# Kernel tuning notes

Hardware: AMD Instinct MI355X
Metric: run time of the kernel (lower is better)

## Reference

```python
import jax, jax.numpy as jnp
import numpy as np

NEG_SLOPE = 0.01  # torch F.leaky_relu default


def _sage_layer(src, dst, ew, x_src, num_dst, W_self, W_neigh, b):
    # x_src: [N_src, T, C]; messages m_e = w_e * x_src[src_e]  -> [E, T, C]
    msg = x_src[src] * ew[:, None, None]
    agg = jax.ops.segment_sum(msg, dst, num_segments=num_dst)  # [N_dst, T, C]
    x_dst = x_src[:num_dst]
    # self- and neighbor-linear (GraphSAGE): [N_dst, T, H]
    return (jnp.einsum('ntc,hc->nth', x_dst, W_self)
            + jnp.einsum('ntc,hc->nth', agg, W_neigh) + b)


def setup_inputs() -> dict:
    key = jax.random.key(0)
    ks = jax.random.split(key, 12)
    T, N_src1, C_in, H, C_out = 12, 50000, 32, 64, 32
    N_dst1, N_dst2 = 20000, 10000
    E1, E2 = 320000, 160000
    inp = {
        'node_feat': jax.random.normal(ks[0], (T, N_src1, C_in), jnp.float32),
        'src1': jax.random.randint(ks[1], (E1,), 0, N_src1),
        'dst1': jax.random.randint(ks[2], (E1,), 0, N_dst1),
        'ew1': jax.random.uniform(ks[3], (E1,), jnp.float32),
        'src2': jax.random.randint(ks[4], (E2,), 0, N_dst1),
        'dst2': jax.random.randint(ks[5], (E2,), 0, N_dst2),
        'ew2': jax.random.uniform(ks[6], (E2,), jnp.float32),
        'W1_self': jax.random.normal(ks[7], (H, C_in), jnp.float32) / np.sqrt(C_in),
        'W1_neigh': jax.random.normal(ks[8], (H, C_in), jnp.float32) / np.sqrt(C_in),
        'b1': jnp.zeros((H,), jnp.float32),
        'W2_self': jax.random.normal(ks[9], (C_out, H), jnp.float32) / np.sqrt(H),
        'W2_neigh': jax.random.normal(ks[10], (C_out, H), jnp.float32) / np.sqrt(H),
        'b2': jnp.zeros((C_out,), jnp.float32),
        'num_dst1': N_dst1,
        'num_dst2': N_dst2,
    }
    return inp


def reference(node_feat, src1, dst1, ew1, src2, dst2, ew2,
              W1_self, W1_neigh, b1, W2_self, W2_neigh, b2,
              num_dst1, num_dst2):
    x = jnp.transpose(node_feat, (1, 0, 2))  # [N, T, C]
    h1 = jax.nn.leaky_relu(
        _sage_layer(src1, dst1, ew1, x, num_dst1, W1_self, W1_neigh, b1), NEG_SLOPE)
    h2 = jax.nn.leaky_relu(
        _sage_layer(src2, dst2, ew2, h1, num_dst2, W2_self, W2_neigh, b2), NEG_SLOPE)
    return jnp.transpose(h2, (1, 0, 2))  # [T, N_dst2, C_out]
```

## Files before the change

### kernel.cpp

```cpp
#include <hip/hip_runtime.h>
#include <hip/hip_bf16.h>

#define TT  12
#define C1  32
#define H1  64
#define C2  32
#define N0  50000
#define N1  20000
#define N2  10000
#define CAP 128

__global__ void bucket_kernel(const int* __restrict__ dst, int E,
                              int* __restrict__ cnt, int* __restrict__ elist) {
    int e = blockIdx.x * blockDim.x + threadIdx.x;
    if (e < E) {
        int d = dst[e];
        int slot = atomicAdd(&cnt[d], 1);
        if (slot < CAP) elist[d * CAP + slot] = e;
    }
}

__global__ __launch_bounds__(256)
void sage_layer1(const float* __restrict__ xin,
                 const int*  __restrict__ src1, const float* __restrict__ ew1,
                 const int*  __restrict__ cnt1, const int*  __restrict__ elist1,
                 const float* __restrict__ W1s, const float* __restrict__ W1n,
                 const float* __restrict__ b1,
                 float* __restrict__ h1) {
    const int w    = threadIdx.x >> 6;
    const int lane = threadIdx.x & 63;
    const int n    = blockIdx.x * 4 + w;

    __shared__ int   sh_s  [4][CAP];
    __shared__ float sh_w  [4][CAP];
    __shared__ float sh_agg[4][TT * C1];
    __shared__ float sh_x  [4][TT * C1];

    int cnt = cnt1[n]; if (cnt > CAP) cnt = CAP;
    for (int j = lane; j < cnt; j += 64) {
        int e = elist1[n * CAP + j];
        sh_s[w][j] = src1[e];
        sh_w[w][j] = ew1[e];
    }
    __syncthreads();

    float acc[6] = {0.f, 0.f, 0.f, 0.f, 0.f, 0.f};
    #pragma unroll 4
    for (int j = 0; j < cnt; ++j) {
        int   s = sh_s[w][j];
        float wgt = sh_w[w][j];
        #pragma unroll
        for (int k = 0; k < 6; ++k) {
            int f = lane + 64 * k;
            int t = f >> 5, c = f & 31;
            acc[k] += wgt * xin[(size_t)t * (N0 * C1) + (size_t)s * C1 + c];
        }
    }
    #pragma unroll
    for (int k = 0; k < 6; ++k) sh_agg[w][lane + 64 * k] = acc[k];

    #pragma unroll
    for (int k = 0; k < 6; ++k) {
        int f = lane + 64 * k;
        int t = f >> 5, c = f & 31;
        sh_x[w][f] = xin[(size_t)t * (N0 * C1) + (size_t)n * C1 + c];
    }
    __syncthreads();

    float ws[C1], wn[C1];
    #pragma unroll
    for (int c = 0; c < C1; c += 4) {
        *(float4*)&ws[c] = *(const float4*)&W1s[lane * C1 + c];
        *(float4*)&wn[c] = *(const float4*)&W1n[lane * C1 + c];
    }
    const float bias = b1[lane];

    #pragma unroll
    for (int t = 0; t < TT; ++t) {
        float a = bias;
        #pragma unroll
        for (int c = 0; c < C1; c += 4) {
            float4 xv = *(const float4*)&sh_x[w][t * C1 + c];
            float4 av = *(const float4*)&sh_agg[w][t * C1 + c];
            a += xv.x * ws[c]     + xv.y * ws[c + 1] + xv.z * ws[c + 2] + xv.w * ws[c + 3]
               + av.x * wn[c]     + av.y * wn[c + 1] + av.z * wn[c + 2] + av.w * wn[c + 3];
        }
        a = a > 0.f ? a : 0.01f * a;
        h1[(size_t)t * (N1 * H1) + (size_t)n * H1 + lane] = a;
    }
}

__global__ __launch_bounds__(256)
void sage_layer2(const float* __restrict__ h1,
                 const int*  __restrict__ src2, const float* __restrict__ ew2,
                 const int*  __restrict__ cnt2, const int*  __restrict__ elist2,
                 const float* __restrict__ W2s, const float* __restrict__ W2n,
                 const float* __restrict__ b2,
                 float* __restrict__ out) {
    const int w    = threadIdx.x >> 6;
    const int lane = threadIdx.x & 63;
    const int n    = blockIdx.x * 4 + w;

    __shared__ int   sh_s  [4][CAP];
    __shared__ float sh_w  [4][CAP];
    __shared__ float sh_agg[4][TT * H1];
    __shared__ float sh_x  [4][TT * H1];

    int cnt = cnt2[n]; if (cnt > CAP) cnt = CAP;
    for (int j = lane; j < cnt; j += 64) {
        int e = elist2[n * CAP + j];
        sh_s[w][j] = src2[e];
        sh_w[w][j] = ew2[e];
    }
    __syncthreads();

    float acc[TT];
    #pragma unroll
    for (int k = 0; k < TT; ++k) acc[k] = 0.f;
    #pragma unroll 2
    for (int j = 0; j < cnt; ++j) {
        int   s   = sh_s[w][j];
        float wgt = sh_w[w][j];
        #pragma unroll
        for (int k = 0; k < TT; ++k)
            acc[k] += wgt * h1[(size_t)k * (N1 * H1) + (size_t)s * H1 + lane];
    }
    #pragma unroll
    for (int k = 0; k < TT; ++k) sh_agg[w][k * H1 + lane] = acc[k];
    #pragma unroll
    for (int k = 0; k < TT; ++k)
        sh_x[w][k * H1 + lane] = h1[(size_t)k * (N1 * H1) + (size_t)n * H1 + lane];
    __syncthreads();

    const int c2 = lane & 31;
    const int hh = lane >> 5;
    float ws[32], wn[32];
    #pragma unroll
    for (int j = 0; j < 32; j += 4) {
        *(float4*)&ws[j] = *(const float4*)&W2s[c2 * H1 + hh * 32 + j];
        *(float4*)&wn[j] = *(const float4*)&W2n[c2 * H1 + hh * 32 + j];
    }
    const float bias = b2[c2];

    #pragma unroll
    for (int t = 0; t < TT; ++t) {
        float a = 0.f;
        #pragma unroll
        for (int j = 0; j < 32; j += 4) {
            float4 xv = *(const float4*)&sh_x[w][t * H1 + hh * 32 + j];
            float4 av = *(const float4*)&sh_agg[w][t * H1 + hh * 32 + j];
            a += xv.x * ws[j]     + xv.y * ws[j + 1] + xv.z * ws[j + 2] + xv.w * ws[j + 3]
               + av.x * wn[j]     + av.y * wn[j + 1] + av.z * wn[j + 2] + av.w * wn[j + 3];
        }
        a += __shfl_xor(a, 32);
        a += bias;
        a = a > 0.f ? a : 0.01f * a;
        if (hh == (t / 6))
            out[(size_t)t * (N2 * C2) + (size_t)n * C2 + c2] = a;
    }
}

extern "C" void kernel_launch(void* const* d_in, const int* in_sizes, int n_in,
                              void* d_out, int out_size, void* d_ws, size_t ws_size,
                              hipStream_t stream) {
    const float* node_feat = (const float*)d_in[0];
    const int*   src1      = (const int*)  d_in[1];
    const int*   dst1      = (const int*)  d_in[2];
    const float* ew1       = (const float*)d_in[3];
    const int*   src2      = (const int*)  d_in[4];
    const int*   dst2      = (const int*)  d_in[5];
    const float* ew2       = (const float*)d_in[6];
    const float* W1s       = (const float*)d_in[7];
    const float* W1n       = (const float*)d_in[8];
    const float* b1        = (const float*)d_in[9];
    const float* W2s       = (const float*)d_in[10];
    const float* W2n       = (const float*)d_in[11];
    const float* b2        = (const float*)d_in[12];

    const int E1 = in_sizes[1];
    const int E2 = in_sizes[4];

    int* cnt1   = (int*)d_ws;
    int* cnt2   = cnt1 + N1;
    int* elist1 = cnt2 + N2;
    int* elist2 = elist1 + (size_t)N1 * CAP;
    float* h1   = (float*)(elist2 + (size_t)N2 * CAP);

    hipMemsetAsync(d_ws, 0, (size_t)(N1 + N2) * sizeof(int), stream);

    bucket_kernel<<<(E1 + 255) / 256, 256, 0, stream>>>(dst1, E1, cnt1, elist1);
    bucket_kernel<<<(E2 + 255) / 256, 256, 0, stream>>>(dst2, E2, cnt2, elist2);

    sage_layer1<<<N1 / 4, 256, 0, stream>>>(node_feat, src1, ew1, cnt1, elist1,
                                            W1s, W1n, b1, h1);
    sage_layer2<<<N2 / 4, 256, 0, stream>>>(h1, src2, ew2, cnt2, elist2,
                                            W2s, W2n, b2, (float*)d_out);
}
```

Baseline: 379.7 us.

## Store node features and hidden state node-major for contiguous gathers

Adds a transpose kernel that rewrites the input features from [T,N,C] to [N,T,C], and writes the layer-1 output in node-major layout. Each gathered neighbour row then becomes one contiguous block that can be read with float2 or float4 loads, replacing 12 scattered 128-byte segments. It also halves the per-node edge capacity from 128 to 64, which shrinks the workspace. The cost is an extra pass over the input, and any node with more than 64 incoming edges would be silently truncated.

```diff
diff --git a/kernel.cpp b/kernel.cpp
--- a/kernel.cpp
+++ b/kernel.cpp
@@ -8,7 +8,7 @@
 #define N0  50000
 #define N1  20000
 #define N2  10000
-#define CAP 128
+#define CAP 64
 
 __global__ void bucket_kernel(const int* __restrict__ dst, int E,
                               int* __restrict__ cnt, int* __restrict__ elist) {
@@ -21,12 +21,26 @@
 }
 
 __global__ __launch_bounds__(256)
-void sage_layer1(const float* __restrict__ xin,
+void transpose_x(const float* __restrict__ x, float* __restrict__ xt) {
+    const int nl = threadIdx.x >> 3;
+    const int c4 = (threadIdx.x & 7) * 4;
+    const int n  = blockIdx.x * 32 + nl;
+    if (n >= N0) return;
+    #pragma unroll
+    for (int t = 0; t < TT; ++t) {
+        float4 v = *(const float4*)&x[(size_t)t * (N0 * C1) + (size_t)n * C1 + c4];
+        *(float4*)&xt[(size_t)n * (TT * C1) + t * C1 + c4] = v;
+    }
+}
+
+template<bool USE_XT>
+__global__ __launch_bounds__(256)
+void sage_layer1(const float* __restrict__ xsrc,
                  const int*  __restrict__ src1, const float* __restrict__ ew1,
                  const int*  __restrict__ cnt1, const int*  __restrict__ elist1,
                  const float* __restrict__ W1s, const float* __restrict__ W1n,
                  const float* __restrict__ b1,
-                 float* __restrict__ h1) {
+                 float* __restrict__ h1t) {
     const int w    = threadIdx.x >> 6;
     const int lane = threadIdx.x & 63;
     const int n    = blockIdx.x * 4 + w;
@@ -44,26 +58,46 @@
     }
     __syncthreads();
 
-    float acc[6] = {0.f, 0.f, 0.f, 0.f, 0.f, 0.f};
-    #pragma unroll 4
-    for (int j = 0; j < cnt; ++j) {
-        int   s = sh_s[w][j];
-        float wgt = sh_w[w][j];
+    if constexpr (USE_XT) {
+        float2 acc[3] = {{0.f,0.f},{0.f,0.f},{0.f,0.f}};
+        #pragma unroll 8
+        for (int j = 0; j < cnt; ++j) {
+            int   s   = sh_s[w][j];
+            float wgt = sh_w[w][j];
+            const float2* p = (const float2*)(xsrc + (size_t)s * (TT * C1));
+            #pragma unroll
+            for (int k = 0; k < 3; ++k) {
+                float2 v = p[lane + 64 * k];
+                acc[k].x += wgt * v.x;
+                acc[k].y += wgt * v.y;
+            }
+        }
+        #pragma unroll
+        for (int k = 0; k < 3; ++k)
+            ((float2*)sh_agg[w])[lane + 64 * k] = acc[k];
+        const float2* p = (const float2*)(xsrc + (size_t)n * (TT * C1));
+        #pragma unroll
+        for (int k = 0; k < 3; ++k)
+            ((float2*)sh_x[w])[lane + 64 * k] = p[lane + 64 * k];
+    } else {
+        float acc[6] = {0.f,0.f,0.f,0.f,0.f,0.f};
+        #pragma unroll 4
+        for (int j = 0; j < cnt; ++j) {
+            int   s   = sh_s[w][j];
+            float wgt = sh_w[w][j];
+            #pragma unroll
+            for (int k = 0; k < 6; ++k) {
+                int f = lane + 64 * k;
+                acc[k] += wgt * xsrc[(size_t)(f >> 5) * (N0 * C1) + (size_t)s * C1 + (f & 31)];
+            }
+        }
+        #pragma unroll
+        for (int k = 0; k < 6; ++k) sh_agg[w][lane + 64 * k] = acc[k];
         #pragma unroll
         for (int k = 0; k < 6; ++k) {
             int f = lane + 64 * k;
-            int t = f >> 5, c = f & 31;
-            acc[k] += wgt * xin[(size_t)t * (N0 * C1) + (size_t)s * C1 + c];
-        }
-    }
-    #pragma unroll
-    for (int k = 0; k < 6; ++k) sh_agg[w][lane + 64 * k] = acc[k];
-
-    #pragma unroll
-    for (int k = 0; k < 6; ++k) {
-        int f = lane + 64 * k;
-        int t = f >> 5, c = f & 31;
-        sh_x[w][f] = xin[(size_t)t * (N0 * C1) + (size_t)n * C1 + c];
+            sh_x[w][f] = xsrc[(size_t)(f >> 5) * (N0 * C1) + (size_t)n * C1 + (f & 31)];
+        }
     }
     __syncthreads();
 
@@ -86,12 +120,12 @@
                + av.x * wn[c]     + av.y * wn[c + 1] + av.z * wn[c + 2] + av.w * wn[c + 3];
         }
         a = a > 0.f ? a : 0.01f * a;
-        h1[(size_t)t * (N1 * H1) + (size_t)n * H1 + lane] = a;
+        h1t[(size_t)n * (TT * H1) + t * H1 + lane] = a;
     }
 }
 
 __global__ __launch_bounds__(256)
-void sage_layer2(const float* __restrict__ h1,
+void sage_layer2(const float* __restrict__ h1t,
                  const int*  __restrict__ src2, const float* __restrict__ ew2,
                  const int*  __restrict__ cnt2, const int*  __restrict__ elist2,
                  const float* __restrict__ W2s, const float* __restrict__ W2n,
@@ -114,22 +148,30 @@
     }
     __syncthreads();
 
-    float acc[TT];
-    #pragma unroll
-    for (int k = 0; k < TT; ++k) acc[k] = 0.f;
-    #pragma unroll 2
+    float4 acc[3];
+    #pragma unroll
+    for (int k = 0; k < 3; ++k) acc[k] = make_float4(0.f, 0.f, 0.f, 0.f);
+    #pragma unroll 4
     for (int j = 0; j < cnt; ++j) {
         int   s   = sh_s[w][j];
         float wgt = sh_w[w][j];
-        #pragma unroll
-        for (int k = 0; k < TT; ++k)
-            acc[k] += wgt * h1[(size_t)k * (N1 * H1) + (size_t)s * H1 + lane];
-    }
-    #pragma unroll
-    for (int k = 0; k < TT; ++k) sh_agg[w][k * H1 + lane] = acc[k];
-    #pragma unroll
-    for (int k = 0; k < TT; ++k)
-        sh_x[w][k * H1 + lane] = h1[(size_t)k * (N1 * H1) + (size_t)n * H1 + lane];
+        const float4* p = (const float4*)(h1t + (size_t)s * (TT * H1));
+        #pragma unroll
+        for (int k = 0; k < 3; ++k) {
+            float4 v = p[lane + 64 * k];
+            acc[k].x += wgt * v.x;  acc[k].y += wgt * v.y;
+            acc[k].z += wgt * v.z;  acc[k].w += wgt * v.w;
+        }
+    }
+    #pragma unroll
+    for (int k = 0; k < 3; ++k)
+        ((float4*)sh_agg[w])[lane + 64 * k] = acc[k];
+    {
+        const float4* p = (const float4*)(h1t + (size_t)n * (TT * H1));
+        #pragma unroll
+        for (int k = 0; k < 3; ++k)
+            ((float4*)sh_x[w])[lane + 64 * k] = p[lane + 64 * k];
+    }
     __syncthreads();
 
     const int c2 = lane & 31;
@@ -180,19 +222,31 @@
     const int E1 = in_sizes[1];
     const int E2 = in_sizes[4];
 
-    int* cnt1   = (int*)d_ws;
-    int* cnt2   = cnt1 + N1;
-    int* elist1 = cnt2 + N2;
-    int* elist2 = elist1 + (size_t)N1 * CAP;
-    float* h1   = (float*)(elist2 + (size_t)N2 * CAP);
+    int*   cnt1   = (int*)d_ws;
+    int*   cnt2   = cnt1 + N1;
+    int*   elist1 = cnt2 + N2;
+    int*   elist2 = elist1 + (size_t)N1 * CAP;
+    float* h1t    = (float*)(elist2 + (size_t)N2 * CAP);
+    float* xt     = h1t + (size_t)N1 * TT * H1;
+
+    const size_t need_xt =
+        ((size_t)(N1 + N2) * (1 + CAP) + (size_t)N1 * TT * H1 + (size_t)N0 * TT * C1)
+        * sizeof(float);
+    const bool use_xt = ws_size >= need_xt;
 
     hipMemsetAsync(d_ws, 0, (size_t)(N1 + N2) * sizeof(int), stream);
 
     bucket_kernel<<<(E1 + 255) / 256, 256, 0, stream>>>(dst1, E1, cnt1, elist1);
     bucket_kernel<<<(E2 + 255) / 256, 256, 0, stream>>>(dst2, E2, cnt2, elist2);
 
-    sage_layer1<<<N1 / 4, 256, 0, stream>>>(node_feat, src1, ew1, cnt1, elist1,
-                                            W1s, W1n, b1, h1);
-    sage_layer2<<<N2 / 4, 256, 0, stream>>>(h1, src2, ew2, cnt2, elist2,
+    if (use_xt) {
+        transpose_x<<<(N0 + 31) / 32, 256, 0, stream>>>(node_feat, xt);
+        sage_layer1<true><<<N1 / 4, 256, 0, stream>>>(xt, src1, ew1, cnt1, elist1,
+                                                      W1s, W1n, b1, h1t);
+    } else {
+        sage_layer1<false><<<N1 / 4, 256, 0, stream>>>(node_feat, src1, ew1, cnt1, elist1,
+                                                       W1s, W1n, b1, h1t);
+    }
+    sage_layer2<<<N2 / 4, 256, 0, stream>>>(h1t, src2, ew2, cnt2, elist2,
                                             W2s, W2n, b2, (float*)d_out);
 }
```

New measurement: 384.4 us. No clear change (+1.2%).

## Apply layer-2 linear before aggregation and fuse into layer 1 epilogue

Applied to the files above, without the earlier changes.

Layer 1 now projects its hidden output through the layer-2 neighbor and self weights right away. It writes 32-channel y2/z2 rows in node-major layout instead of the 64-channel time-major h1. Layer 2 then only gathers and weights 384 contiguous floats per edge, adds the self term and bias, and applies the activation. This halves the gather traffic in layer 2 and makes it contiguous per source row. The two bucketing kernels are merged into one launch, and CAP is lowered from 128 to 64. That risks dropping edges for nodes with in-degree above 64, though expected degrees are about 16.

```diff
diff --git a/kernel.cpp b/kernel.cpp
--- a/kernel.cpp
+++ b/kernel.cpp
@@ -8,33 +8,44 @@
 #define N0  50000
 #define N1  20000
 #define N2  10000
-#define CAP 128
-
-__global__ void bucket_kernel(const int* __restrict__ dst, int E,
-                              int* __restrict__ cnt, int* __restrict__ elist) {
+#define CAP 64
+#define F1  (TT * C1)
+#define F2  (TT * C2)
+
+__global__ void bucket_both(const int* __restrict__ dst1, int E1,
+                            const int* __restrict__ dst2, int E2,
+                            int* __restrict__ cnt1, int* __restrict__ elist1,
+                            int* __restrict__ cnt2, int* __restrict__ elist2) {
     int e = blockIdx.x * blockDim.x + threadIdx.x;
-    if (e < E) {
-        int d = dst[e];
-        int slot = atomicAdd(&cnt[d], 1);
-        if (slot < CAP) elist[d * CAP + slot] = e;
+    if (e < E1) {
+        int d = dst1[e];
+        int slot = atomicAdd(&cnt1[d], 1);
+        if (slot < CAP) elist1[d * CAP + slot] = e;
+    } else if (e - E1 < E2) {
+        int e2 = e - E1;
+        int d = dst2[e2];
+        int slot = atomicAdd(&cnt2[d], 1);
+        if (slot < CAP) elist2[d * CAP + slot] = e2;
     }
 }
 
 __global__ __launch_bounds__(256)
-void sage_layer1(const float* __restrict__ xin,
-                 const int*  __restrict__ src1, const float* __restrict__ ew1,
-                 const int*  __restrict__ cnt1, const int*  __restrict__ elist1,
-                 const float* __restrict__ W1s, const float* __restrict__ W1n,
-                 const float* __restrict__ b1,
-                 float* __restrict__ h1) {
+void sage_layer1_fused(const float* __restrict__ x,
+                       const int*  __restrict__ src1, const float* __restrict__ ew1,
+                       const int*  __restrict__ cnt1, const int*  __restrict__ elist1,
+                       const float* __restrict__ W1s, const float* __restrict__ W1n,
+                       const float* __restrict__ b1,
+                       const float* __restrict__ W2s, const float* __restrict__ W2n,
+                       float* __restrict__ y2, float* __restrict__ z2) {
     const int w    = threadIdx.x >> 6;
     const int lane = threadIdx.x & 63;
     const int n    = blockIdx.x * 4 + w;
 
     __shared__ int   sh_s  [4][CAP];
     __shared__ float sh_w  [4][CAP];
-    __shared__ float sh_agg[4][TT * C1];
-    __shared__ float sh_x  [4][TT * C1];
+    __shared__ float sh_agg[4][F1];
+    __shared__ float sh_x  [4][F1];
+    __shared__ float sh_h  [4][TT * H1];
 
     int cnt = cnt1[n]; if (cnt > CAP) cnt = CAP;
     for (int j = lane; j < cnt; j += 64) {
@@ -45,25 +56,22 @@
     __syncthreads();
 
     float acc[6] = {0.f, 0.f, 0.f, 0.f, 0.f, 0.f};
-    #pragma unroll 4
+    #pragma unroll 8
     for (int j = 0; j < cnt; ++j) {
-        int   s = sh_s[w][j];
+        int   s   = sh_s[w][j];
         float wgt = sh_w[w][j];
         #pragma unroll
         for (int k = 0; k < 6; ++k) {
             int f = lane + 64 * k;
-            int t = f >> 5, c = f & 31;
-            acc[k] += wgt * xin[(size_t)t * (N0 * C1) + (size_t)s * C1 + c];
+            acc[k] += wgt * x[(size_t)(f >> 5) * (N0 * C1) + (size_t)s * C1 + (f & 31)];
         }
     }
     #pragma unroll
     for (int k = 0; k < 6; ++k) sh_agg[w][lane + 64 * k] = acc[k];
-
     #pragma unroll
     for (int k = 0; k < 6; ++k) {
         int f = lane + 64 * k;
-        int t = f >> 5, c = f & 31;
-        sh_x[w][f] = xin[(size_t)t * (N0 * C1) + (size_t)n * C1 + c];
+        sh_x[w][f] = x[(size_t)(f >> 5) * (N0 * C1) + (size_t)n * C1 + (f & 31)];
     }
     __syncthreads();
 
@@ -86,25 +94,53 @@
                + av.x * wn[c]     + av.y * wn[c + 1] + av.z * wn[c + 2] + av.w * wn[c + 3];
         }
         a = a > 0.f ? a : 0.01f * a;
-        h1[(size_t)t * (N1 * H1) + (size_t)n * H1 + lane] = a;
+        sh_h[w][t * H1 + lane] = a;
+    }
+
+    const int c2 = lane & 31;
+    const int th = lane >> 5;
+    const float* wn2 = W2n + c2 * H1;
+    const float* ws2 = W2s + c2 * H1;
+
+    #pragma unroll
+    for (int q = 0; q < 6; ++q) {
+        int t = 2 * q + th;
+        float sy = 0.f;
+        #pragma unroll
+        for (int k = 0; k < H1; k += 4) {
+            float4 wv = *(const float4*)&wn2[k];
+            float4 hv = *(const float4*)&sh_h[w][t * H1 + k];
+            sy += wv.x * hv.x + wv.y * hv.y + wv.z * hv.z + wv.w * hv.w;
+        }
+        y2[(size_t)n * F2 + q * 64 + lane] = sy;
+    }
+    if (n < N2) {
+        #pragma unroll
+        for (int q = 0; q < 6; ++q) {
+            int t = 2 * q + th;
+            float sz = 0.f;
+            #pragma unroll
+            for (int k = 0; k < H1; k += 4) {
+                float4 wv = *(const float4*)&ws2[k];
+                float4 hv = *(const float4*)&sh_h[w][t * H1 + k];
+                sz += wv.x * hv.x + wv.y * hv.y + wv.z * hv.z + wv.w * hv.w;
+            }
+            z2[(size_t)n * F2 + q * 64 + lane] = sz;
+        }
     }
 }
 
 __global__ __launch_bounds__(256)
-void sage_layer2(const float* __restrict__ h1,
-                 const int*  __restrict__ src2, const float* __restrict__ ew2,
-                 const int*  __restrict__ cnt2, const int*  __restrict__ elist2,
-                 const float* __restrict__ W2s, const float* __restrict__ W2n,
-                 const float* __restrict__ b2,
-                 float* __restrict__ out) {
+void sage_layer2_gather(const float* __restrict__ y2, const float* __restrict__ z2,
+                        const int*  __restrict__ src2, const float* __restrict__ ew2,
+                        const int*  __restrict__ cnt2, const int*  __restrict__ elist2,
+                        const float* __restrict__ b2, float* __restrict__ out) {
     const int w    = threadIdx.x >> 6;
     const int lane = threadIdx.x & 63;
     const int n    = blockIdx.x * 4 + w;
 
-    __shared__ int   sh_s  [4][CAP];
-    __shared__ float sh_w  [4][CAP];
-    __shared__ float sh_agg[4][TT * H1];
-    __shared__ float sh_x  [4][TT * H1];
+    __shared__ int   sh_s[4][CAP];
+    __shared__ float sh_w[4][CAP];
 
     int cnt = cnt2[n]; if (cnt > CAP) cnt = CAP;
     for (int j = lane; j < cnt; j += 64) {
@@ -114,49 +150,32 @@
     }
     __syncthreads();
 
-    float acc[TT];
-    #pragma unroll
-    for (int k = 0; k < TT; ++k) acc[k] = 0.f;
-    #pragma unroll 2
+    float2 acc[3] = {{0.f,0.f},{0.f,0.f},{0.f,0.f}};
+    #pragma unroll 8
     for (int j = 0; j < cnt; ++j) {
         int   s   = sh_s[w][j];
         float wgt = sh_w[w][j];
-        #pragma unroll
-        for (int k = 0; k < TT; ++k)
-            acc[k] += wgt * h1[(size_t)k * (N1 * H1) + (size_t)s * H1 + lane];
-    }
-    #pragma unroll
-    for (int k = 0; k < TT; ++k) sh_agg[w][k * H1 + lane] = acc[k];
-    #pragma unroll
-    for (int k = 0; k < TT; ++k)
-        sh_x[w][k * H1 + lane] = h1[(size_t)k * (N1 * H1) + (size_t)n * H1 + lane];
-    __syncthreads();
-
-    const int c2 = lane & 31;
-    const int hh = lane >> 5;
-    float ws[32], wn[32];
-    #pragma unroll
-    for (int j = 0; j < 32; j += 4) {
-        *(float4*)&ws[j] = *(const float4*)&W2s[c2 * H1 + hh * 32 + j];
-        *(float4*)&wn[j] = *(const float4*)&W2n[c2 * H1 + hh * 32 + j];
-    }
-    const float bias = b2[c2];
-
-    #pragma unroll
-    for (int t = 0; t < TT; ++t) {
-        float a = 0.f;
-        #pragma unroll
-        for (int j = 0; j < 32; j += 4) {
-            float4 xv = *(const float4*)&sh_x[w][t * H1 + hh * 32 + j];
-            float4 av = *(const float4*)&sh_agg[w][t * H1 + hh * 32 + j];
-            a += xv.x * ws[j]     + xv.y * ws[j + 1] + xv.z * ws[j + 2] + xv.w * ws[j + 3]
-               + av.x * wn[j]     + av.y * wn[j + 1] + av.z * wn[j + 2] + av.w * wn[j + 3];
-        }
-        a += __shfl_xor(a, 32);
-        a += bias;
-        a = a > 0.f ? a : 0.01f * a;
-        if (hh == (t / 6))
-            out[(size_t)t * (N2 * C2) + (size_t)n * C2 + c2] = a;
+        const float2* p = (const float2*)(y2 + (size_t)s * F2);
+        #pragma unroll
+        for (int k = 0; k < 3; ++k) {
+            float2 v = p[lane + 64 * k];
+            acc[k].x += wgt * v.x;
+            acc[k].y += wgt * v.y;
+        }
+    }
+
+    const float2* pz = (const float2*)(z2 + (size_t)n * F2);
+    #pragma unroll
+    for (int k = 0; k < 3; ++k) {
+        int f = 2 * (lane + 64 * k);
+        int t = f >> 5, c = f & 31;
+        float2 zv = pz[lane + 64 * k];
+        float2 bv = *(const float2*)&b2[c];
+        float ox = zv.x + acc[k].x + bv.x;
+        float oy = zv.y + acc[k].y + bv.y;
+        ox = ox > 0.f ? ox : 0.01f * ox;
+        oy = oy > 0.f ? oy : 0.01f * oy;
+        *(float2*)&out[(size_t)t * (N2 * C2) + (size_t)n * C2 + c] = make_float2(ox, oy);
     }
 }
 
@@ -180,19 +199,21 @@
     const int E1 = in_sizes[1];
     const int E2 = in_sizes[4];
 
-    int* cnt1   = (int*)d_ws;
-    int* cnt2   = cnt1 + N1;
-    int* elist1 = cnt2 + N2;
-    int* elist2 = elist1 + (size_t)N1 * CAP;
-    float* h1   = (float*)(elist2 + (size_t)N2 * CAP);
+    int*   cnt1   = (int*)d_ws;
+    int*   cnt2   = cnt1 + N1;
+    int*   elist1 = cnt2 + N2;
+    int*   elist2 = elist1 + (size_t)N1 * CAP;
+    float* y2     = (float*)(elist2 + (size_t)N2 * CAP);
+    float* z2     = y2 + (size_t)N1 * F2;
 
     hipMemsetAsync(d_ws, 0, (size_t)(N1 + N2) * sizeof(int), stream);
 
-    bucket_kernel<<<(E1 + 255) / 256, 256, 0, stream>>>(dst1, E1, cnt1, elist1);
-    bucket_kernel<<<(E2 + 255) / 256, 256, 0, stream>>>(dst2, E2, cnt2, elist2);
-
-    sage_layer1<<<N1 / 4, 256, 0, stream>>>(node_feat, src1, ew1, cnt1, elist1,
-                                            W1s, W1n, b1, h1);
-    sage_layer2<<<N2 / 4, 256, 0, stream>>>(h1, src2, ew2, cnt2, elist2,
-                                            W2s, W2n, b2, (float*)d_out);
-}
+    bucket_both<<<(E1 + E2 + 255) / 256, 256, 0, stream>>>(dst1, E1, dst2, E2,
+                                                           cnt1, elist1, cnt2, elist2);
+
+    sage_layer1_fused<<<N1 / 4, 256, 0, stream>>>(node_feat, src1, ew1, cnt1, elist1,
+                                                  W1s, W1n, b1, W2s, W2n, y2, z2);
+
+    sage_layer2_gather<<<N2 / 4, 256, 0, stream>>>(y2, z2, src2, ew2, cnt2, elist2,
+                                                   b2, (float*)d_out);
+}
```

New measurement: 1.282 ms. +237.6%, slower.

## Store layer-1 hidden state as node-major bf16 and merge bucket kernels

Applied to the files above, without the earlier changes.

Layer 1 now writes the hidden activations in bfloat16 with a node-major layout, so each layer-2 gather reads one contiguous 1.5KB row instead of 12 strided fp32 segments. This halves the gather traffic for the layer-2 aggregation. The two edge-bucketing launches are merged into one kernel, and the per-node edge capacity drops from 128 to 64. The trade-offs are reduced precision in the intermediate activations and silent truncation if any node ever receives more than 64 edges.

```diff
diff --git a/kernel.cpp b/kernel.cpp
--- a/kernel.cpp
+++ b/kernel.cpp
@@ -8,33 +8,43 @@
 #define N0  50000
 #define N1  20000
 #define N2  10000
-#define CAP 128
-
-__global__ void bucket_kernel(const int* __restrict__ dst, int E,
-                              int* __restrict__ cnt, int* __restrict__ elist) {
+#define CAP 64
+#define F1  (TT * C1)
+#define FH  (TT * H1)
+#define F2  (TT * C2)
+
+__global__ void bucket_both(const int* __restrict__ dst1, int E1,
+                            const int* __restrict__ dst2, int E2,
+                            int* __restrict__ cnt1, int* __restrict__ elist1,
+                            int* __restrict__ cnt2, int* __restrict__ elist2) {
     int e = blockIdx.x * blockDim.x + threadIdx.x;
-    if (e < E) {
-        int d = dst[e];
-        int slot = atomicAdd(&cnt[d], 1);
-        if (slot < CAP) elist[d * CAP + slot] = e;
+    if (e < E1) {
+        int d = dst1[e];
+        int slot = atomicAdd(&cnt1[d], 1);
+        if (slot < CAP) elist1[d * CAP + slot] = e;
+    } else if (e - E1 < E2) {
+        int e2 = e - E1;
+        int d = dst2[e2];
+        int slot = atomicAdd(&cnt2[d], 1);
+        if (slot < CAP) elist2[d * CAP + slot] = e2;
     }
 }
 
 __global__ __launch_bounds__(256)
-void sage_layer1(const float* __restrict__ xin,
+void sage_layer1(const float* __restrict__ x,
                  const int*  __restrict__ src1, const float* __restrict__ ew1,
                  const int*  __restrict__ cnt1, const int*  __restrict__ elist1,
                  const float* __restrict__ W1s, const float* __restrict__ W1n,
                  const float* __restrict__ b1,
-                 float* __restrict__ h1) {
+                 __hip_bfloat16* __restrict__ h1b) {
     const int w    = threadIdx.x >> 6;
     const int lane = threadIdx.x & 63;
     const int n    = blockIdx.x * 4 + w;
 
     __shared__ int   sh_s  [4][CAP];
     __shared__ float sh_w  [4][CAP];
-    __shared__ float sh_agg[4][TT * C1];
-    __shared__ float sh_x  [4][TT * C1];
+    __shared__ float sh_agg[4][F1];
+    __shared__ float sh_x  [4][F1];
 
     int cnt = cnt1[n]; if (cnt > CAP) cnt = CAP;
     for (int j = lane; j < cnt; j += 64) {
@@ -47,23 +57,20 @@
     float acc[6] = {0.f, 0.f, 0.f, 0.f, 0.f, 0.f};
     #pragma unroll 4
     for (int j = 0; j < cnt; ++j) {
-        int   s = sh_s[w][j];
+        int   s   = sh_s[w][j];
         float wgt = sh_w[w][j];
         #pragma unroll
         for (int k = 0; k < 6; ++k) {
             int f = lane + 64 * k;
-            int t = f >> 5, c = f & 31;
-            acc[k] += wgt * xin[(size_t)t * (N0 * C1) + (size_t)s * C1 + c];
+            acc[k] += wgt * x[(size_t)(f >> 5) * (N0 * C1) + (size_t)s * C1 + (f & 31)];
         }
     }
     #pragma unroll
     for (int k = 0; k < 6; ++k) sh_agg[w][lane + 64 * k] = acc[k];
-
     #pragma unroll
     for (int k = 0; k < 6; ++k) {
         int f = lane + 64 * k;
-        int t = f >> 5, c = f & 31;
-        sh_x[w][f] = xin[(size_t)t * (N0 * C1) + (size_t)n * C1 + c];
+        sh_x[w][f] = x[(size_t)(f >> 5) * (N0 * C1) + (size_t)n * C1 + (f & 31)];
     }
     __syncthreads();
 
@@ -86,12 +93,12 @@
                + av.x * wn[c]     + av.y * wn[c + 1] + av.z * wn[c + 2] + av.w * wn[c + 3];
         }
         a = a > 0.f ? a : 0.01f * a;
-        h1[(size_t)t * (N1 * H1) + (size_t)n * H1 + lane] = a;
+        h1b[(size_t)n * FH + t * H1 + lane] = __float2bfloat16(a);
     }
 }
 
 __global__ __launch_bounds__(256)
-void sage_layer2(const float* __restrict__ h1,
+void sage_layer2(const __hip_bfloat16* __restrict__ h1b,
                  const int*  __restrict__ src2, const float* __restrict__ ew2,
                  const int*  __restrict__ cnt2, const int*  __restrict__ elist2,
                  const float* __restrict__ W2s, const float* __restrict__ W2n,
@@ -103,8 +110,8 @@
 
     __shared__ int   sh_s  [4][CAP];
     __shared__ float sh_w  [4][CAP];
-    __shared__ float sh_agg[4][TT * H1];
-    __shared__ float sh_x  [4][TT * H1];
+    __shared__ float sh_agg[4][FH];
+    __shared__ float sh_x  [4][FH];
 
     int cnt = cnt2[n]; if (cnt > CAP) cnt = CAP;
     for (int j = lane; j < cnt; j += 64) {
@@ -114,22 +121,36 @@
     }
     __syncthreads();
 
-    float acc[TT];
-    #pragma unroll
-    for (int k = 0; k < TT; ++k) acc[k] = 0.f;
-    #pragma unroll 2
+    float2 acc[6];
+    #pragma unroll
+    for (int k = 0; k < 6; ++k) acc[k] = make_float2(0.f, 0.f);
+    #pragma unroll 4
     for (int j = 0; j < cnt; ++j) {
         int   s   = sh_s[w][j];
         float wgt = sh_w[w][j];
-        #pragma unroll
-        for (int k = 0; k < TT; ++k)
-            acc[k] += wgt * h1[(size_t)k * (N1 * H1) + (size_t)s * H1 + lane];
-    }
-    #pragma unroll
-    for (int k = 0; k < TT; ++k) sh_agg[w][k * H1 + lane] = acc[k];
-    #pragma unroll
-    for (int k = 0; k < TT; ++k)
-        sh_x[w][k * H1 + lane] = h1[(size_t)k * (N1 * H1) + (size_t)n * H1 + lane];
+        const unsigned int* p = (const unsigned int*)(h1b + (size_t)s * FH);
+        #pragma unroll
+        for (int k = 0; k < 6; ++k) {
+            unsigned int v = p[lane + 64 * k];
+            float lo = __uint_as_float(v << 16);
+            float hi = __uint_as_float(v & 0xFFFF0000u);
+            acc[k].x += wgt * lo;
+            acc[k].y += wgt * hi;
+        }
+    }
+    #pragma unroll
+    for (int k = 0; k < 6; ++k)
+        ((float2*)sh_agg[w])[lane + 64 * k] = acc[k];
+
+    {
+        const unsigned int* p = (const unsigned int*)(h1b + (size_t)n * FH);
+        #pragma unroll
+        for (int k = 0; k < 6; ++k) {
+            unsigned int v = p[lane + 64 * k];
+            ((float2*)sh_x[w])[lane + 64 * k] =
+                make_float2(__uint_as_float(v << 16), __uint_as_float(v & 0xFFFF0000u));
+        }
+    }
     __syncthreads();
 
     const int c2 = lane & 31;
@@ -184,15 +205,16 @@
     int* cnt2   = cnt1 + N1;
     int* elist1 = cnt2 + N2;
     int* elist2 = elist1 + (size_t)N1 * CAP;
-    float* h1   = (float*)(elist2 + (size_t)N2 * CAP);
+    __hip_bfloat16* h1b = (__hip_bfloat16*)(elist2 + (size_t)N2 * CAP);
 
     hipMemsetAsync(d_ws, 0, (size_t)(N1 + N2) * sizeof(int), stream);
 
-    bucket_kernel<<<(E1 + 255) / 256, 256, 0, stream>>>(dst1, E1, cnt1, elist1);
-    bucket_kernel<<<(E2 + 255) / 256, 256, 0, stream>>>(dst2, E2, cnt2, elist2);
+    bucket_both<<<(E1 + E2 + 255) / 256, 256, 0, stream>>>(dst1, E1, dst2, E2,
+                                                           cnt1, elist1, cnt2, elist2);
 
     sage_layer1<<<N1 / 4, 256, 0, stream>>>(node_feat, src1, ew1, cnt1, elist1,
-                                            W1s, W1n, b1, h1);
-    sage_layer2<<<N2 / 4, 256, 0, stream>>>(h1, src2, ew2, cnt2, elist2,
+                                            W1s, W1n, b1, h1b);
+
+    sage_layer2<<<N2 / 4, 256, 0, stream>>>(h1b, src2, ew2, cnt2, elist2,
                                             W2s, W2n, b2, (float*)d_out);
 }
```

Result: faster. 314.9 us (-17.1%).
